# Optimization experiments

Measured on AMD Instinct MI355X. Metric: run time of the kernel, lower is better.

Reference implementation:

```python
import jax, jax.numpy as jnp
import numpy as np

NUM_USERS = 50000
NUM_ITEMS = 50000
NUM_CATS = 500
LATENT_DIM = 64
N_LAYERS = 3
N_EDGES = 500000
NNZ_G = 1000000
NNZ_GX = 2000000
BATCH = 8192
N_NODES = NUM_USERS + NUM_ITEMS


def _spmm(rows, cols, vals, x, n_out):
    # sparse COO matmul: out[r] += vals * x[c]
    return jax.ops.segment_sum(vals[:, None] * x[cols], rows, num_segments=n_out)


def setup_inputs() -> dict:
    key = jax.random.key(0)
    ks = jax.random.split(key, 14)
    return {
        "user_emb": 0.1 * jax.random.normal(ks[0], (NUM_USERS, LATENT_DIM), jnp.float32),
        "item_emb": 0.1 * jax.random.normal(ks[1], (NUM_ITEMS, LATENT_DIM), jnp.float32),
        "cat_emb": 0.1 * jax.random.normal(ks[2], (NUM_CATS, 2 * LATENT_DIM), jnp.float32),
        "g_vals": jax.random.uniform(ks[3], (NNZ_G,), jnp.float32),
        "gx_vals": jax.random.uniform(ks[4], (NNZ_GX,), jnp.float32),
        "g_rows": jax.random.randint(ks[5], (NNZ_G,), 0, N_NODES, jnp.int32),
        "g_cols": jax.random.randint(ks[6], (NNZ_G,), 0, N_NODES, jnp.int32),
        "gx_rows": jax.random.randint(ks[7], (NNZ_GX,), 0, N_EDGES, jnp.int32),
        "gx_cols": jax.random.randint(ks[8], (NNZ_GX,), 0, N_EDGES, jnp.int32),
        "train_users": jax.random.randint(ks[9], (N_EDGES,), 0, NUM_USERS, jnp.int32),
        "train_items": jax.random.randint(ks[10], (N_EDGES,), 0, NUM_ITEMS, jnp.int32),
        "item_to_category": jax.random.randint(ks[11], (NUM_ITEMS,), 0, NUM_CATS, jnp.int32),
        "users": jax.random.randint(ks[12], (BATCH,), 0, NUM_USERS, jnp.int32),
        "items": jax.random.randint(ks[13], (BATCH,), 0, NUM_ITEMS, jnp.int32),
    }


def _computer(user_emb, item_emb, cat_emb, g_rows, g_cols, g_vals,
              gx_rows, gx_cols, gx_vals, train_users, train_items, item_to_category):
    D = LATENT_DIM
    all_emb = jnp.concatenate([user_emb, item_emb], axis=0)  # [N, D]
    item_nodes = NUM_USERS + train_items  # [E]
    # degree = bincount over train_users and shifted train_items
    degree = (jnp.zeros((N_NODES,), all_emb.dtype)
              .at[train_users].add(1.0)
              .at[item_nodes].add(1.0))
    edge_cat = cat_emb[item_to_category[train_items]]  # [E, 2D]
    embs = []
    for i in range(N_LAYERS):
        all_emb = _spmm(g_rows, g_cols, g_vals, all_emb, N_NODES)  # [N, D]
        # edge features: user||item concat, +category emb on first layer
        feat = jnp.concatenate([all_emb[train_users], all_emb[item_nodes]], axis=-1)  # [E, 2D]
        if i == 0:
            feat = feat + edge_cat
        feat = _spmm(gx_rows, gx_cols, gx_vals, feat, N_EDGES)  # [E, 2D]
        # scatter edge halves back to nodes, degree-normalize, residual average
        upd = (jnp.zeros_like(all_emb)
               .at[train_users].add(feat[:, :D])
               .at[item_nodes].add(feat[:, D:]))
        upd = upd / (degree[:, None] + 1e-9)
        all_emb = (upd + all_emb) * 0.5
        embs.append(all_emb)
    light_out = jnp.mean(jnp.stack(embs, axis=1), axis=1)  # mean over layers 1..L
    return light_out[:NUM_USERS], light_out[NUM_USERS:]


def reference(user_emb, item_emb, cat_emb, g_vals, gx_vals, g_rows, g_cols,
              gx_rows, gx_cols, train_users, train_items, item_to_category,
              users, items):
    all_users, all_items = _computer(user_emb, item_emb, cat_emb,
                                     g_rows, g_cols, g_vals,
                                     gx_rows, gx_cols, gx_vals,
                                     train_users, train_items, item_to_category)
    u = all_users[users]   # [B, D]
    it = all_items[items]  # [B, D]
    gamma = jnp.sum(u * it, axis=1)  # [B]
    return gamma
```

## Files before the change

kernel.cpp:

```cpp
#include <hip/hip_runtime.h>

#define NUM_USERS 50000
#define NUM_ITEMS 50000
#define NUM_CATS  500
#define D         64
#define N_LAYERS  3
#define N_EDGES   500000
#define NNZ_G     1000000
#define NNZ_GX    2000000
#define BATCH     8192
#define N_NODES   (NUM_USERS + NUM_ITEMS)

#define BKT_SHIFT 4
#define BKT_W     16
#define NBKT      (N_NODES / BKT_W)

#define SB_SHIFT  9
#define SB_W      512
#define NSB       ((N_NODES + SB_W - 1) / SB_W)
#define P1_K      15
#define P1_TILE   (256 * P1_K)
#define P1_REC    (2 * P1_TILE)

__device__ __forceinline__ unsigned bf16rne(float f) {
    unsigned u = __float_as_uint(f);
    return (u + 0x7FFFu + ((u >> 16) & 1u)) >> 16;
}
__device__ __forceinline__ void bf16x8_to_f8(uint4 w, float* r) {
    r[0] = __uint_as_float(w.x << 16); r[1] = __uint_as_float(w.x & 0xFFFF0000u);
    r[2] = __uint_as_float(w.y << 16); r[3] = __uint_as_float(w.y & 0xFFFF0000u);
    r[4] = __uint_as_float(w.z << 16); r[5] = __uint_as_float(w.z & 0xFFFF0000u);
    r[6] = __uint_as_float(w.w << 16); r[7] = __uint_as_float(w.w & 0xFFFF0000u);
}
__device__ __forceinline__ uint4 f8_to_bf16x8(const float* r) {
    uint4 w;
    w.x = bf16rne(r[0]) | (bf16rne(r[1]) << 16);
    w.y = bf16rne(r[2]) | (bf16rne(r[3]) << 16);
    w.z = bf16rne(r[4]) | (bf16rne(r[5]) << 16);
    w.w = bf16rne(r[6]) | (bf16rne(r[7]) << 16);
    return w;
}

__global__ void deg_kernel(const int* __restrict__ tu, const int* __restrict__ ti,
                           float* __restrict__ deg) {
    int e = blockIdx.x * blockDim.x + threadIdx.x;
    if (e >= N_EDGES) return;
    unsafeAtomicAdd(deg + tu[e], 1.0f);
    unsafeAtomicAdd(deg + NUM_USERS + ti[e], 1.0f);
}

__global__ void dinv_kernel(float* __restrict__ deg) {
    int n = blockIdx.x * blockDim.x + threadIdx.x;
    if (n < N_NODES) deg[n] = 1.0f / (deg[n] + 1e-9f);
}

__global__ void init_x_kernel(const float* __restrict__ ue, const float* __restrict__ ie,
                              ushort* __restrict__ xb) {
    int i4 = blockIdx.x * blockDim.x + threadIdx.x;
    if (i4 >= N_NODES * D / 4) return;
    const int half = NUM_USERS * D / 4;
    float4 v = (i4 < half) ? ((const float4*)ue)[i4] : ((const float4*)ie)[i4 - half];
    uint2 p;
    p.x = bf16rne(v.x) | (bf16rne(v.y) << 16);
    p.y = bf16rne(v.z) | (bf16rne(v.w) << 16);
    ((uint2*)xb)[i4] = p;
}

__global__ void histsb_c_kernel(const int* __restrict__ gx_rows,
                                const int* __restrict__ tu, const int* __restrict__ ti,
                                int* __restrict__ cnt) {
    __shared__ int h[NSB];
    for (int i = threadIdx.x; i < NSB; i += blockDim.x) h[i] = 0;
    __syncthreads();
    int stride = gridDim.x * blockDim.x;
    for (int j = blockIdx.x * blockDim.x + threadIdx.x; j < NNZ_GX; j += stride) {
        int r = gx_rows[j];
        atomicAdd(h + (tu[r] >> SB_SHIFT), 1);
        atomicAdd(h + ((NUM_USERS + ti[r]) >> SB_SHIFT), 1);
    }
    __syncthreads();
    for (int i = threadIdx.x; i < NSB; i += blockDim.x)
        if (h[i]) atomicAdd(cnt + i, h[i]);
}

__global__ void scansb_kernel(const int* __restrict__ cnt, int* __restrict__ off,
                              int* __restrict__ cur, int* __restrict__ row_sentinel) {
    if (threadIdx.x == 0) {
        int run = 0;
        for (int i = 0; i < NSB; ++i) { off[i] = run; cur[i] = run; run += cnt[i]; }
        off[NSB] = run;
        row_sentinel[0] = run;
    }
}

__global__ void __launch_bounds__(256) p1c_kernel(
        const int* __restrict__ gx_rows, const int* __restrict__ gx_cols,
        const float* __restrict__ gx_vals,
        const int* __restrict__ tu, const int* __restrict__ ti,
        const int* __restrict__ i2c,
        int* __restrict__ sbcur, int2* __restrict__ out) {
    __shared__ int2 recs[P1_REC];
    __shared__ int h[NSB], base[NSB], cur[NSB];
    int t = threadIdx.x;
    for (int i = t; i < NSB; i += 256) { h[i] = 0; cur[i] = 0; }
    __syncthreads();
    int tb = blockIdx.x * P1_TILE;
    #pragma unroll
    for (int k = 0; k < P1_K; ++k) {
        int l = t + k * 256;
        int j = tb + l;
        if (j < NNZ_GX) {
            int r = gx_rows[j], c = gx_cols[j];
            unsigned vb = bf16rne(gx_vals[j]);
            int tur = tu[r], tir = ti[r], tuc = tu[c], tic = ti[c];
            int cat = i2c[tic];
            int ylo = (int)(vb << 16) | (cat << 1);
            unsigned dstu = (unsigned)tur;           int srcu = tuc;
            unsigned dsti = (unsigned)(NUM_USERS + tir); int srci = NUM_USERS + tic;
            recs[2 * l] = make_int2((int)((dstu << 15) | (unsigned)(srcu & 0x7FFF)),
                                    ylo | (((srcu >> 15) & 3) << 10));
            recs[2 * l + 1] = make_int2((int)((dsti << 15) | (unsigned)(srci & 0x7FFF)),
                                        ylo | (((srci >> 15) & 3) << 10) | 1);
            atomicAdd(h + (int)(dstu >> SB_SHIFT), 1);
            atomicAdd(h + (int)(dsti >> SB_SHIFT), 1);
        }
    }
    __syncthreads();
    if (t < NSB) base[t] = atomicAdd(sbcur + t, h[t]);
    __syncthreads();
    int rem = NNZ_GX - tb;
    int nrec = 2 * (rem < P1_TILE ? rem : P1_TILE);
    for (int s = t; s < nrec; s += 256) {
        int2 rec = recs[s];
        int bkt = (int)(((unsigned)rec.x) >> 24);
        int p = base[bkt] + atomicAdd(cur + bkt, 1);
        out[p] = rec;
    }
}

__global__ void __launch_bounds__(512) p2c_kernel(
        const int* __restrict__ sboff, const int2* __restrict__ raw,
        int2* __restrict__ sorted, int* __restrict__ rowC) {
    int b = blockIdx.x;
    int beg = sboff[b], end = sboff[b + 1];
    __shared__ int h[SB_W], cur[SB_W];
    int t = threadIdx.x;
    h[t] = 0;
    __syncthreads();
    for (int i = beg + t; i < end; i += 512)
        atomicAdd(h + (int)((((unsigned)raw[i].x) >> 15) & (SB_W - 1)), 1);
    __syncthreads();
    int cnt = h[t];
    for (int o = 1; o < SB_W; o <<= 1) {
        int tmp = (t >= o) ? h[t - o] : 0;
        __syncthreads();
        h[t] += tmp;
        __syncthreads();
    }
    int excl = h[t] - cnt;
    cur[t] = beg + excl;
    int node = b * SB_W + t;
    if (node < N_NODES) rowC[node] = beg + excl;
    __syncthreads();
    for (int i = beg + t; i < end; i += 512) {
        int2 e = raw[i];
        unsigned rx = (unsigned)e.x;
        int dl = (int)((rx >> 15) & (SB_W - 1));
        int src = (int)(rx & 0x7FFF) | (((e.y >> 10) & 3) << 15);
        int p = atomicAdd(cur + dl, 1);
        sorted[p] = make_int2((src << 10) | (e.y & 0x3FF), e.y & 0xFFFF0000);
    }
}

__global__ void histg_kernel(const int* __restrict__ g_rows, int* __restrict__ cnt) {
    __shared__ int h[NBKT];
    for (int i = threadIdx.x; i < NBKT; i += blockDim.x) h[i] = 0;
    __syncthreads();
    int stride = gridDim.x * blockDim.x;
    for (int e = blockIdx.x * blockDim.x + threadIdx.x; e < NNZ_G; e += stride)
        atomicAdd(h + (g_rows[e] >> BKT_SHIFT), 1);
    __syncthreads();
    for (int i = threadIdx.x; i < NBKT; i += blockDim.x)
        if (h[i]) atomicAdd(cnt + i, h[i]);
}

__global__ void scang_kernel(const int* __restrict__ cnt, int* __restrict__ off,
                             int* __restrict__ cur, int* __restrict__ row) {
    __shared__ int sums[1024];
    const int T = 1024;
    const int strip = (NBKT + T - 1) / T;
    int t = threadIdx.x;
    int beg = t * strip;
    int end = beg + strip; if (end > NBKT) end = NBKT;
    int s = 0;
    for (int i = beg; i < end; ++i) s += cnt[i];
    sums[t] = s;
    __syncthreads();
    if (t == 0) {
        int run = 0;
        for (int i = 0; i < T; ++i) { int v = sums[i]; sums[i] = run; run += v; }
        off[NBKT] = run;
        row[N_NODES] = run;
    }
    __syncthreads();
    int run = sums[t];
    for (int i = beg; i < end; ++i) { off[i] = run; cur[i] = run; run += cnt[i]; }
}

__global__ void append_g_kernel(const int* __restrict__ g_rows, const int* __restrict__ g_cols,
                                const float* __restrict__ g_vals,
                                int* __restrict__ cur, int2* __restrict__ edges) {
    int e = blockIdx.x * blockDim.x + threadIdx.x;
    if (e >= NNZ_G) return;
    int dst = g_rows[e];
    int p = atomicAdd(cur + (dst >> BKT_SHIFT), 1);
    edges[p] = make_int2(((dst & (BKT_W - 1)) << 17) | g_cols[e], __float_as_int(g_vals[e]));
}

__global__ void sort_g_kernel(const int* __restrict__ off, const int2* __restrict__ raw,
                              int2* __restrict__ sorted, int* __restrict__ rowG) {
    int b = blockIdx.x;
    int base = off[b], end = off[b + 1];
    __shared__ int hist[BKT_W], cur[BKT_W], scn[BKT_W];
    if (threadIdx.x < BKT_W) hist[threadIdx.x] = 0;
    __syncthreads();
    for (int i = base + threadIdx.x; i < end; i += blockDim.x)
        atomicAdd(hist + ((raw[i].x >> 17) & 15), 1);
    __syncthreads();
    if (threadIdx.x == 0) {
        int run = 0;
        for (int k = 0; k < BKT_W; ++k) { scn[k] = run; cur[k] = run; run += hist[k]; }
    }
    __syncthreads();
    if (threadIdx.x < BKT_W) rowG[b * BKT_W + threadIdx.x] = base + scn[threadIdx.x];
    for (int i = base + threadIdx.x; i < end; i += blockDim.x) {
        int2 e = raw[i];
        int dl = (e.x >> 17) & 15;
        int p = atomicAdd(cur + dl, 1);
        sorted[base + p] = make_int2((e.x & 0x1FFFF) << 6, e.y);
    }
}

__global__ void pull_g_kernel(const int* __restrict__ row, const int2* __restrict__ edges,
                              const ushort* __restrict__ xb, ushort* __restrict__ tb) {
    int wave = (blockIdx.x * blockDim.x + threadIdx.x) >> 6;
    int lane = threadIdx.x & 63;
    if (wave >= N_NODES) return;
    int g = lane >> 3;
    int s = lane & 7;
    int beg = row[wave], end = row[wave + 1];
    float acc[8] = {0.f, 0.f, 0.f, 0.f, 0.f, 0.f, 0.f, 0.f};
    #pragma unroll 2
    for (int i = beg + g; i < end; i += 8) {
        int2 e = edges[i];
        float v = __int_as_float(e.y);
        uint4 w = *(const uint4*)(xb + e.x + s * 8);
        float xv[8];
        bf16x8_to_f8(w, xv);
        #pragma unroll
        for (int d = 0; d < 8; ++d) acc[d] += v * xv[d];
    }
    #pragma unroll
    for (int d = 0; d < 8; ++d) {
        acc[d] += __shfl_xor(acc[d], 8, 64);
        acc[d] += __shfl_xor(acc[d], 16, 64);
        acc[d] += __shfl_xor(acc[d], 32, 64);
    }
    if (lane < 8) {
        uint4 p = f8_to_bf16x8(acc);
        *(uint4*)(tb + (size_t)wave * D + lane * 8) = p;
    }
}

template <int LAYER0>
__global__ void pull_c_fused(const int* __restrict__ row, const int2* __restrict__ edges,
                             const float* __restrict__ catbase,
                             const ushort* __restrict__ tb,
                             const float* __restrict__ dinv,
                             ushort* __restrict__ xb, float* __restrict__ accb) {
    int wave = (blockIdx.x * blockDim.x + threadIdx.x) >> 6;
    int lane = threadIdx.x & 63;
    if (wave >= N_NODES) return;
    int g = lane >> 3;
    int s = lane & 7;
    int beg = row[wave], end = row[wave + 1];
    float acc[8] = {0.f, 0.f, 0.f, 0.f, 0.f, 0.f, 0.f, 0.f};
    #pragma unroll 2
    for (int i = beg + g; i < end; i += 8) {
        int2 e = edges[i];
        float v = __int_as_float(e.y);
        int src = e.x >> 10;
        uint4 w = *(const uint4*)(tb + (size_t)src * D + s * 8);
        float xv[8];
        bf16x8_to_f8(w, xv);
        if (LAYER0) {
            int code = e.x & 1023;
            const float* cb = catbase + (code >> 1) * (2 * D) + ((code & 1) << 6) + s * 8;
            float4 c0 = *(const float4*)cb;
            float4 c1 = *(const float4*)(cb + 4);
            xv[0] += c0.x; xv[1] += c0.y; xv[2] += c0.z; xv[3] += c0.w;
            xv[4] += c1.x; xv[5] += c1.y; xv[6] += c1.z; xv[7] += c1.w;
        }
        #pragma unroll
        for (int d = 0; d < 8; ++d) acc[d] += v * xv[d];
    }
    #pragma unroll
    for (int d = 0; d < 8; ++d) {
        acc[d] += __shfl_xor(acc[d], 8, 64);
        acc[d] += __shfl_xor(acc[d], 16, 64);
        acc[d] += __shfl_xor(acc[d], 32, 64);
    }
    if (lane < 8) {
        float di = dinv[wave];
        size_t o = (size_t)wave * D + lane * 8;
        uint4 tw = *(const uint4*)(tb + o);
        float tv[8];
        bf16x8_to_f8(tw, tv);
        float nx[8];
        #pragma unroll
        for (int d = 0; d < 8; ++d) nx[d] = (acc[d] * di + tv[d]) * 0.5f;
        *(uint4*)(xb + o) = f8_to_bf16x8(nx);
        float4 a0 = *(const float4*)(accb + o);
        float4 a1 = *(const float4*)(accb + o + 4);
        a0.x += nx[0]; a0.y += nx[1]; a0.z += nx[2]; a0.w += nx[3];
        a1.x += nx[4]; a1.y += nx[5]; a1.z += nx[6]; a1.w += nx[7];
        *(float4*)(accb + o) = a0;
        *(float4*)(accb + o + 4) = a1;
    }
}

__global__ void gamma_kernel(const int* __restrict__ users, const int* __restrict__ items,
                             const float* __restrict__ acc, float* __restrict__ out) {
    int wave = (blockIdx.x * blockDim.x + threadIdx.x) >> 6;
    int lane = threadIdx.x & 63;
    if (wave >= BATCH) return;
    int u = users[wave], it = items[wave];
    float p = acc[(size_t)u * D + lane] * acc[(size_t)(NUM_USERS + it) * D + lane];
#pragma unroll
    for (int off = 32; off > 0; off >>= 1) p += __shfl_down(p, off, 64);
    if (lane == 0) out[wave] = p * (1.0f / 9.0f);
}

extern "C" void kernel_launch(void* const* d_in, const int* in_sizes, int n_in,
                              void* d_out, int out_size, void* d_ws, size_t ws_size,
                              hipStream_t stream) {
    const float* user_emb = (const float*)d_in[0];
    const float* item_emb = (const float*)d_in[1];
    const float* cat_emb  = (const float*)d_in[2];
    const float* g_vals   = (const float*)d_in[3];
    const float* gx_vals  = (const float*)d_in[4];
    const int* g_rows  = (const int*)d_in[5];
    const int* g_cols  = (const int*)d_in[6];
    const int* gx_rows = (const int*)d_in[7];
    const int* gx_cols = (const int*)d_in[8];
    const int* train_users = (const int*)d_in[9];
    const int* train_items = (const int*)d_in[10];
    const int* i2c   = (const int*)d_in[11];
    const int* users = (const int*)d_in[12];
    const int* items = (const int*)d_in[13];
    float* out = (float*)d_out;

    char* ws = (char*)d_ws;
    size_t off = 0;
    auto alloc = [&](size_t bytes) -> void* {
        void* p = ws + off;
        off += (bytes + 255) & ~(size_t)255;
        return p;
    };
    const size_t NB = (size_t)N_NODES * D * sizeof(float);
    const size_t NBH = (size_t)N_NODES * D * sizeof(ushort);
    ushort* xb   = (ushort*)alloc(NBH);
    ushort* tb   = (ushort*)alloc(NBH);
    float*  accb = (float*)alloc(NB);
    float*  dinv = (float*)alloc((size_t)N_NODES * sizeof(float));
    int*  sbhC  = (int*)alloc((size_t)NSB * sizeof(int));
    int*  sboffC= (int*)alloc((size_t)(NSB + 1) * sizeof(int));
    int*  sbcurC= (int*)alloc((size_t)NSB * sizeof(int));
    int*  cntG  = (int*)alloc((size_t)NBKT * sizeof(int));
    int*  offG  = (int*)alloc((size_t)(NBKT + 1) * sizeof(int));
    int*  curG  = (int*)alloc((size_t)NBKT * sizeof(int));
    int*  rowC  = (int*)alloc((size_t)(N_NODES + 1) * sizeof(int));
    int*  rowG  = (int*)alloc((size_t)(N_NODES + 1) * sizeof(int));
    int2* edgeCr = (int2*)alloc((size_t)2 * NNZ_GX * sizeof(int2));
    int2* edgeCs = (int2*)alloc((size_t)2 * NNZ_GX * sizeof(int2));
    int2* edgeGr = (int2*)alloc((size_t)NNZ_G * sizeof(int2));
    int2* edgeGs = (int2*)alloc((size_t)NNZ_G * sizeof(int2));

    hipMemsetAsync(accb, 0, NB, stream);
    hipMemsetAsync(dinv, 0, (size_t)N_NODES * sizeof(float), stream);
    hipMemsetAsync(sbhC, 0, (size_t)NSB * sizeof(int), stream);
    hipMemsetAsync(cntG, 0, (size_t)NBKT * sizeof(int), stream);

    init_x_kernel<<<(N_NODES * D / 4 + 255) / 256, 256, 0, stream>>>(user_emb, item_emb, xb);
    deg_kernel<<<(N_EDGES + 255) / 256, 256, 0, stream>>>(train_users, train_items, dinv);
    dinv_kernel<<<(N_NODES + 255) / 256, 256, 0, stream>>>(dinv);

    histsb_c_kernel<<<256, 256, 0, stream>>>(gx_rows, train_users, train_items, sbhC);
    scansb_kernel<<<1, 64, 0, stream>>>(sbhC, sboffC, sbcurC, rowC + N_NODES);
    p1c_kernel<<<(NNZ_GX + P1_TILE - 1) / P1_TILE, 256, 0, stream>>>(
        gx_rows, gx_cols, gx_vals, train_users, train_items, i2c, sbcurC, edgeCr);
    p2c_kernel<<<NSB, 512, 0, stream>>>(sboffC, edgeCr, edgeCs, rowC);

    histg_kernel<<<256, 256, 0, stream>>>(g_rows, cntG);
    scang_kernel<<<1, 1024, 0, stream>>>(cntG, offG, curG, rowG);
    append_g_kernel<<<(NNZ_G + 255) / 256, 256, 0, stream>>>(g_rows, g_cols, g_vals,
                                                             curG, edgeGr);
    sort_g_kernel<<<NBKT, 256, 0, stream>>>(offG, edgeGr, edgeGs, rowG);

    const int pull_grid = (N_NODES * 64 + 255) / 256;
    for (int layer = 0; layer < N_LAYERS; ++layer) {
        pull_g_kernel<<<pull_grid, 256, 0, stream>>>(rowG, edgeGs, xb, tb);
        if (layer == 0)
            pull_c_fused<1><<<pull_grid, 256, 0, stream>>>(rowC, edgeCs, cat_emb, tb,
                                                           dinv, xb, accb);
        else
            pull_c_fused<0><<<pull_grid, 256, 0, stream>>>(rowC, edgeCs, cat_emb, tb,
                                                           dinv, xb, accb);
    }

    gamma_kernel<<<(BATCH * 64 + 255) / 256, 256, 0, stream>>>(users, items, accb, out);
}
```

Baseline: 781.1 us.

## Map two nodes per wavefront in pull kernels and shrink p1c tile

The pull kernels now give each graph node 32 lanes instead of a full 64-lane wavefront, so two nodes share a wave and the reduction drops one shuffle stage. Average degree is about 10 for G and 40 for the combined graph, so many of the 64 lanes were idle and this is meant to raise lane utilisation. The grid is halved to match. Separately, the p1c binning kernel uses a smaller tile and splits the user and item records into two halves of shared memory, cutting LDS use per block so more blocks can be resident. The 32-lane node groups rely on the width-64 xor shuffles by 8 and 16 staying inside each half-wave, which they do.

```diff
diff --git a/kernel.cpp b/kernel.cpp
--- a/kernel.cpp
+++ b/kernel.cpp
@@ -18,9 +18,8 @@
 #define SB_SHIFT  9
 #define SB_W      512
 #define NSB       ((N_NODES + SB_W - 1) / SB_W)
-#define P1_K      15
+#define P1_K      8
 #define P1_TILE   (256 * P1_K)
-#define P1_REC    (2 * P1_TILE)
 
 __device__ __forceinline__ unsigned bf16rne(float f) {
     unsigned u = __float_as_uint(f);
@@ -99,7 +98,7 @@
         const int* __restrict__ tu, const int* __restrict__ ti,
         const int* __restrict__ i2c,
         int* __restrict__ sbcur, int2* __restrict__ out) {
-    __shared__ int2 recs[P1_REC];
+    __shared__ int2 recs[2 * P1_TILE];
     __shared__ int h[NSB], base[NSB], cur[NSB];
     int t = threadIdx.x;
     for (int i = t; i < NSB; i += 256) { h[i] = 0; cur[i] = 0; }
@@ -117,10 +116,10 @@
             int ylo = (int)(vb << 16) | (cat << 1);
             unsigned dstu = (unsigned)tur;           int srcu = tuc;
             unsigned dsti = (unsigned)(NUM_USERS + tir); int srci = NUM_USERS + tic;
-            recs[2 * l] = make_int2((int)((dstu << 15) | (unsigned)(srcu & 0x7FFF)),
-                                    ylo | (((srcu >> 15) & 3) << 10));
-            recs[2 * l + 1] = make_int2((int)((dsti << 15) | (unsigned)(srci & 0x7FFF)),
-                                        ylo | (((srci >> 15) & 3) << 10) | 1);
+            recs[l] = make_int2((int)((dstu << 15) | (unsigned)(srcu & 0x7FFF)),
+                                ylo | (((srcu >> 15) & 3) << 10));
+            recs[P1_TILE + l] = make_int2((int)((dsti << 15) | (unsigned)(srci & 0x7FFF)),
+                                          ylo | (((srci >> 15) & 3) << 10) | 1);
             atomicAdd(h + (int)(dstu >> SB_SHIFT), 1);
             atomicAdd(h + (int)(dsti >> SB_SHIFT), 1);
         }
@@ -129,11 +128,15 @@
     if (t < NSB) base[t] = atomicAdd(sbcur + t, h[t]);
     __syncthreads();
     int rem = NNZ_GX - tb;
-    int nrec = 2 * (rem < P1_TILE ? rem : P1_TILE);
-    for (int s = t; s < nrec; s += 256) {
+    int nv = rem < P1_TILE ? rem : P1_TILE;
+    for (int s = t; s < nv; s += 256) {
         int2 rec = recs[s];
         int bkt = (int)(((unsigned)rec.x) >> 24);
         int p = base[bkt] + atomicAdd(cur + bkt, 1);
+        out[p] = rec;
+        rec = recs[P1_TILE + s];
+        bkt = (int)(((unsigned)rec.x) >> 24);
+        p = base[bkt] + atomicAdd(cur + bkt, 1);
         out[p] = rec;
     }
 }
@@ -243,15 +246,15 @@
 
 __global__ void pull_g_kernel(const int* __restrict__ row, const int2* __restrict__ edges,
                               const ushort* __restrict__ xb, ushort* __restrict__ tb) {
-    int wave = (blockIdx.x * blockDim.x + threadIdx.x) >> 6;
-    int lane = threadIdx.x & 63;
-    if (wave >= N_NODES) return;
-    int g = lane >> 3;
-    int s = lane & 7;
-    int beg = row[wave], end = row[wave + 1];
+    int node = (blockIdx.x * blockDim.x + threadIdx.x) >> 5;
+    int l32 = threadIdx.x & 31;
+    if (node >= N_NODES) return;
+    int g = l32 >> 3;
+    int s = l32 & 7;
+    int beg = row[node], end = row[node + 1];
     float acc[8] = {0.f, 0.f, 0.f, 0.f, 0.f, 0.f, 0.f, 0.f};
     #pragma unroll 2
-    for (int i = beg + g; i < end; i += 8) {
+    for (int i = beg + g; i < end; i += 4) {
         int2 e = edges[i];
         float v = __int_as_float(e.y);
         uint4 w = *(const uint4*)(xb + e.x + s * 8);
@@ -264,11 +267,10 @@
     for (int d = 0; d < 8; ++d) {
         acc[d] += __shfl_xor(acc[d], 8, 64);
         acc[d] += __shfl_xor(acc[d], 16, 64);
-        acc[d] += __shfl_xor(acc[d], 32, 64);
-    }
-    if (lane < 8) {
+    }
+    if (l32 < 8) {
         uint4 p = f8_to_bf16x8(acc);
-        *(uint4*)(tb + (size_t)wave * D + lane * 8) = p;
+        *(uint4*)(tb + (size_t)node * D + s * 8) = p;
     }
 }
 
@@ -278,15 +280,15 @@
                              const ushort* __restrict__ tb,
                              const float* __restrict__ dinv,
                              ushort* __restrict__ xb, float* __restrict__ accb) {
-    int wave = (blockIdx.x * blockDim.x + threadIdx.x) >> 6;
-    int lane = threadIdx.x & 63;
-    if (wave >= N_NODES) return;
-    int g = lane >> 3;
-    int s = lane & 7;
-    int beg = row[wave], end = row[wave + 1];
+    int node = (blockIdx.x * blockDim.x + threadIdx.x) >> 5;
+    int l32 = threadIdx.x & 31;
+    if (node >= N_NODES) return;
+    int g = l32 >> 3;
+    int s = l32 & 7;
+    int beg = row[node], end = row[node + 1];
     float acc[8] = {0.f, 0.f, 0.f, 0.f, 0.f, 0.f, 0.f, 0.f};
     #pragma unroll 2
-    for (int i = beg + g; i < end; i += 8) {
+    for (int i = beg + g; i < end; i += 4) {
         int2 e = edges[i];
         float v = __int_as_float(e.y);
         int src = e.x >> 10;
@@ -308,11 +310,10 @@
     for (int d = 0; d < 8; ++d) {
         acc[d] += __shfl_xor(acc[d], 8, 64);
         acc[d] += __shfl_xor(acc[d], 16, 64);
-        acc[d] += __shfl_xor(acc[d], 32, 64);
-    }
-    if (lane < 8) {
-        float di = dinv[wave];
-        size_t o = (size_t)wave * D + lane * 8;
+    }
+    if (l32 < 8) {
+        float di = dinv[node];
+        size_t o = (size_t)node * D + s * 8;
         uint4 tw = *(const uint4*)(tb + o);
         float tv[8];
         bf16x8_to_f8(tw, tv);
@@ -407,7 +408,7 @@
                                                              curG, edgeGr);
     sort_g_kernel<<<NBKT, 256, 0, stream>>>(offG, edgeGr, edgeGs, rowG);
 
-    const int pull_grid = (N_NODES * 64 + 255) / 256;
+    const int pull_grid = (N_NODES * 32 + 255) / 256;
     for (int layer = 0; layer < N_LAYERS; ++layer) {
         pull_g_kernel<<<pull_grid, 256, 0, stream>>>(rowG, edgeGs, xb, tb);
         if (layer == 0)
```

Result: faster. 714.7 us (-8.5%).
